# Performance work log

Hardware: AMD Instinct MI355X
Metric: run time of the kernel (lower is better)

The kernel has to match this reference:

```python
import jax, jax.numpy as jnp
import numpy as np

HIDDEN = 1024
INTER = 2816
NUM_EXPERTS = 8
TOP_K = 2
NUM_TASK_EXPERTS = 4
NUM_GENERALISTS = 2
NUM_TASKS = 8
BSZ, SEQ = 4, 2048
NEG = -1e9


def setup_inputs() -> dict:
    key = jax.random.key(0)
    ks = jax.random.split(key, 8)
    s = 1.0 / np.sqrt(HIDDEN)
    si = 1.0 / np.sqrt(INTER)
    return {
        "hidden_states": jax.random.normal(ks[0], (BSZ, SEQ, HIDDEN), jnp.float32),
        "task_id": 3,
        "task_emb": jax.random.normal(ks[1], (NUM_TASKS, HIDDEN), jnp.float32) * 0.02,
        "task_router_w": jax.random.uniform(ks[2], (NUM_EXPERTS, HIDDEN), jnp.float32, -s, s),
        "gate_weight": jax.random.uniform(ks[3], (NUM_EXPERTS, HIDDEN), jnp.float32, -s, s),
        "gate_proj": jax.random.uniform(ks[4], (NUM_EXPERTS, INTER, HIDDEN), jnp.float32, -s, s),
        "up_proj": jax.random.uniform(ks[5], (NUM_EXPERTS, INTER, HIDDEN), jnp.float32, -s, s),
        "down_proj": jax.random.uniform(ks[6], (NUM_EXPERTS, HIDDEN, INTER), jnp.float32, -si, si),
    }


def reference(hidden_states, task_id, task_emb, task_router_w, gate_weight,
              gate_proj, up_proj, down_proj):
    bsz, seq, dim = hidden_states.shape
    E, K = NUM_EXPERTS, TOP_K

    # ---- task-level routing: pick active experts ----
    task_vec = task_emb[task_id]                         # [d]
    task_scores = task_router_w @ task_vec               # [E]
    _, task_idx = jax.lax.top_k(task_scores, NUM_TASK_EXPERTS)
    gen_idx = jnp.arange(E - NUM_GENERALISTS, E)
    active_mask = jnp.zeros((E,), bool).at[task_idx].set(True).at[gen_idx].set(True)

    # ---- token-level gating over active experts (masked full softmax == subset softmax) ----
    gate_input = (hidden_states + task_vec).reshape(-1, dim)      # [N, d]
    logits = gate_input @ gate_weight.T                            # [N, E]
    scores = jax.nn.softmax(jnp.where(active_mask, logits, NEG), axis=-1)
    topk_gates, topk_idx = jax.lax.top_k(scores, K)                # [N, K]
    topk_gates = topk_gates / (topk_gates.sum(-1, keepdims=True) + 1e-6)

    # per-token per-expert combine weight: [N, E]
    comb = (jax.nn.one_hot(topk_idx, E, dtype=topk_gates.dtype) * topk_gates[..., None]).sum(1)

    # ---- expert MLPs (SwiGLU), dense-per-expert then weighted combine ----
    tokens = hidden_states.reshape(-1, dim)                        # [N, d]
    y = jnp.zeros_like(tokens)
    for e in range(E):
        h = jax.nn.silu(tokens @ gate_proj[e].T) * (tokens @ up_proj[e].T)  # [N, I]
        y = y + comb[:, e:e + 1] * (h @ down_proj[e].T)
    return y.reshape(bsz, seq, dim)
```

## Files before the change

### kernel.cpp

```cpp
#include <hip/hip_runtime.h>

#define HIDDEN 1024
#define INTER 2816
#define NE 8
#define NTOK 8192
#define CPAD 32

typedef _Float16 f16;
typedef f16 f16x8 __attribute__((ext_vector_type(8)));
typedef f16 f16x4v __attribute__((ext_vector_type(4)));
typedef float f32x4 __attribute__((ext_vector_type(4)));

typedef __attribute__((address_space(3))) void lds_void;
typedef __attribute__((address_space(1))) void glb_void;

__device__ __forceinline__ void gl_lds16(const void* g, void* l) {
  __builtin_amdgcn_global_load_lds((const glb_void*)g, (lds_void*)l, 16, 0, 0);
}

__device__ __forceinline__ f32x4 mfma16(f16x8 a, f16x8 b, f32x4 c) {
  return __builtin_amdgcn_mfma_f32_16x16x32_f16(a, b, c, 0, 0, 0);
}

__device__ __forceinline__ f16x8 cvt8(float4 a, float4 b) {
  f16x8 v;
  v[0] = (f16)a.x; v[1] = (f16)a.y; v[2] = (f16)a.z; v[3] = (f16)a.w;
  v[4] = (f16)b.x; v[5] = (f16)b.y; v[6] = (f16)b.z; v[7] = (f16)b.w;
  return v;
}

__global__ void k_route(const float* __restrict__ task_emb,
                        const int* __restrict__ task_id_p,
                        const float* __restrict__ trw,
                        int* __restrict__ mask, int* __restrict__ counts) {
  __shared__ float sc[NE];
  const int tid = threadIdx.x;
  counts[tid] = 0;
  const float* tv = task_emb + (size_t)task_id_p[0] * HIDDEN;
  const int e = tid >> 5, l = tid & 31;
  float p = 0.f;
  for (int k = l; k < HIDDEN; k += 32) p += trw[e * HIDDEN + k] * tv[k];
  for (int o = 16; o > 0; o >>= 1) p += __shfl_down(p, o, 32);
  if (l == 0) sc[e] = p;
  __syncthreads();
  if (tid == 0) {
    int m[NE];
    bool used[NE];
    for (int i = 0; i < NE; ++i) { m[i] = 0; used[i] = false; }
    for (int it = 0; it < 4; ++it) {
      float best = -1e30f; int bi = 0;
      for (int i = 0; i < NE; ++i)
        if (!used[i] && sc[i] > best) { best = sc[i]; bi = i; }
      used[bi] = true; m[bi] = 1;
    }
    m[NE - 2] = 1; m[NE - 1] = 1;
    for (int i = 0; i < NE; ++i) mask[i] = m[i];
  }
}

__global__ __launch_bounds__(256) void k_gate(
    const float* __restrict__ x, const float* __restrict__ task_emb,
    const int* __restrict__ task_id_p, const float* __restrict__ gw,
    const int* __restrict__ mask, int* __restrict__ counts,
    int* __restrict__ tok_list, int* __restrict__ tk_e,
    int* __restrict__ tk_pos, float* __restrict__ tk_w,
    f16* __restrict__ X16) {
  const int tid = threadIdx.x;
  const int g = tid >> 3, l8 = tid & 7;
  const int t = blockIdx.x * 32 + g;
  const float4* tv4 = (const float4*)(task_emb + (size_t)task_id_p[0] * HIDDEN);
  const float4* xr4 = (const float4*)(x + (size_t)t * HIDDEN);
  const float4* gw4 = (const float4*)gw;

  float acc[NE];
#pragma unroll
  for (int e = 0; e < NE; ++e) acc[e] = 0.f;
#pragma unroll 4
  for (int it = 0; it < 32; ++it) {
    const int idx4 = it * 8 + l8;
    float4 xv = xr4[idx4];
    f16x4v h4;
    h4[0] = (f16)xv.x; h4[1] = (f16)xv.y; h4[2] = (f16)xv.z; h4[3] = (f16)xv.w;
    *(f16x4v*)(X16 + (size_t)t * HIDDEN + idx4 * 4) = h4;
    float4 tvv = tv4[idx4];
    const float gx = xv.x + tvv.x, gy = xv.y + tvv.y;
    const float gz = xv.z + tvv.z, gwv = xv.w + tvv.w;
#pragma unroll
    for (int e = 0; e < NE; ++e) {
      float4 w = gw4[e * 256 + idx4];
      acc[e] += gx * w.x + gy * w.y + gz * w.z + gwv * w.w;
    }
  }
#pragma unroll
  for (int e = 0; e < NE; ++e) {
    acc[e] += __shfl_down(acc[e], 4, 8);
    acc[e] += __shfl_down(acc[e], 2, 8);
    acc[e] += __shfl_down(acc[e], 1, 8);
  }

  __shared__ int s_e0[32], s_e1[32], s_r0[32], s_r1[32], s_base[NE];
  __shared__ float s_w0[32], s_w1[32];

  if (l8 == 0) {
    float mx = -1e30f;
    for (int e = 0; e < NE; ++e) if (mask[e] && acc[e] > mx) mx = acc[e];
    float pr[NE]; float s = 0.f;
    for (int e = 0; e < NE; ++e) {
      pr[e] = mask[e] ? expf(acc[e] - mx) : 0.f;
      s += pr[e];
    }
    int i0 = 0; float v0 = -1.f;
    for (int e = 0; e < NE; ++e) if (pr[e] > v0) { v0 = pr[e]; i0 = e; }
    int i1 = (i0 == 0) ? 1 : 0; float v1 = -1.f;
    for (int e = 0; e < NE; ++e) if (e != i0 && pr[e] > v1) { v1 = pr[e]; i1 = e; }
    float g0 = v0 / s, g1 = v1 / s;
    float d = g0 + g1 + 1e-6f;
    s_e0[g] = i0; s_e1[g] = i1;
    s_w0[g] = g0 / d; s_w1[g] = g1 / d;
  }
  __syncthreads();
  if (tid == 0) {
    int cnt[NE];
#pragma unroll
    for (int e = 0; e < NE; ++e) cnt[e] = 0;
    for (int i = 0; i < 32; ++i) {
      s_r0[i] = cnt[s_e0[i]]++;
      s_r1[i] = cnt[s_e1[i]]++;
    }
    for (int e = 0; e < NE; ++e)
      s_base[e] = cnt[e] ? atomicAdd(&counts[e * CPAD], cnt[e]) : 0;
  }
  __syncthreads();
  if (l8 == 0) {
    const int e0 = s_e0[g], e1 = s_e1[g];
    const int p0 = s_base[e0] + s_r0[g];
    const int p1 = s_base[e1] + s_r1[g];
    tok_list[e0 * NTOK + p0] = t;
    tok_list[e1 * NTOK + p1] = t;
    tk_e[t] = e0; tk_e[NTOK + t] = e1;
    tk_pos[t] = p0; tk_pos[NTOK + t] = p1;
    tk_w[t] = s_w0[g]; tk_w[NTOK + t] = s_w1[g];
  }
}

__global__ __launch_bounds__(256) void k_wcvt(
    const float* __restrict__ Wg, const float* __restrict__ Wu,
    const float* __restrict__ Wd, const int* __restrict__ mask,
    f16* __restrict__ Wg16, f16* __restrict__ Wu16, f16* __restrict__ Wd16) {
  const int e = blockIdx.z;
  if (!mask[e]) return;
  const int sel = blockIdx.y;
  const float* src = sel == 0 ? Wg : (sel == 1 ? Wu : Wd);
  f16* dst = sel == 0 ? Wg16 : (sel == 1 ? Wu16 : Wd16);
  const size_t i = (size_t)e * INTER * HIDDEN +
                   ((size_t)blockIdx.x * 256 + threadIdx.x) * 8;
  const float4* s4 = (const float4*)(src + i);
  float4 a = s4[0], b = s4[1];
  *(f16x8*)(dst + i) = cvt8(a, b);
}

__global__ __launch_bounds__(256, 2) void k_gateup16(
    const f16* __restrict__ X16, const f16* __restrict__ Wg16,
    const f16* __restrict__ Wu16, const int* __restrict__ counts,
    const int* __restrict__ tok_list, f16* __restrict__ H) {
  const int e = blockIdx.z;
  int ne = 0, pbase = 0;
#pragma unroll
  for (int i = 0; i < NE; ++i) {
    int c = counts[i * CPAD];
    if (i < e) pbase += c;
    if (i == e) ne = c;
  }
  const int m0 = blockIdx.x * 128;
  if (m0 >= ne) return;
  const int n0 = blockIdx.y * 64;

  __shared__ __align__(16) f16 As[128][64];
  __shared__ __align__(16) f16 Bg[64][64];
  __shared__ __align__(16) f16 Bu[64][64];
  __shared__ int toks[128];

  const int tid = threadIdx.x;
  if (tid < 128) {
    int r = m0 + tid;
    toks[tid] = tok_list[e * NTOK + (r < ne ? r : ne - 1)];
  }
  __syncthreads();

  const int row8 = tid >> 3;
  const int sw = ((tid & 7) ^ (row8 & 7)) * 8;
  const f16* asrc[4];
#pragma unroll
  for (int l = 0; l < 4; ++l)
    asrc[l] = X16 + (size_t)toks[l * 32 + row8] * HIDDEN + sw;
  f16* aldst0 = &As[0][0] + tid * 8;
  const size_t ewoff = (size_t)e * INTER * HIDDEN;
  const f16* gsrc0 = Wg16 + ewoff + (size_t)(n0 + row8) * HIDDEN + sw;
  const f16* usrc0 = Wu16 + ewoff + (size_t)(n0 + row8) * HIDDEN + sw;
  f16* gdst0 = &Bg[0][0] + tid * 8;
  f16* udst0 = &Bu[0][0] + tid * 8;

  const int lane = tid & 63;
  const int wave = tid >> 6;
  const int wm = (wave >> 1) * 64;
  const int wn = (wave & 1) * 32;
  const int l15 = lane & 15, grp = lane >> 4;

  const f32x4 zf = {0.f, 0.f, 0.f, 0.f};
  f32x4 accg[4][2], accu[4][2];
#pragma unroll
  for (int i = 0; i < 4; ++i)
#pragma unroll
    for (int j = 0; j < 2; ++j) { accg[i][j] = zf; accu[i][j] = zf; }

#pragma unroll 1
  for (int k0 = 0; k0 < HIDDEN; k0 += 64) {
#pragma unroll
    for (int l = 0; l < 4; ++l)
      gl_lds16(asrc[l] + k0, aldst0 + l * 2048);
    gl_lds16(gsrc0 + k0, gdst0);
    gl_lds16(gsrc0 + k0 + 32 * HIDDEN, gdst0 + 2048);
    gl_lds16(usrc0 + k0, udst0);
    gl_lds16(usrc0 + k0 + 32 * HIDDEN, udst0 + 2048);
    __syncthreads();

#pragma unroll
    for (int h = 0; h < 2; ++h) {
      const int pc = (((h * 4 + grp) ^ (l15 & 7)) << 4);
      f16x8 af[4];
#pragma unroll
      for (int i = 0; i < 4; ++i)
        af[i] = *(const f16x8*)((const char*)&As[0][0] +
                                (wm + i * 16 + l15) * 128 + pc);
      f16x8 bg[2], bu[2];
#pragma unroll
      for (int j = 0; j < 2; ++j) {
        bg[j] = *(const f16x8*)((const char*)&Bg[0][0] +
                                (wn + j * 16 + l15) * 128 + pc);
        bu[j] = *(const f16x8*)((const char*)&Bu[0][0] +
                                (wn + j * 16 + l15) * 128 + pc);
      }
#pragma unroll
      for (int i = 0; i < 4; ++i)
#pragma unroll
        for (int j = 0; j < 2; ++j) {
          accg[i][j] = mfma16(af[i], bg[j], accg[i][j]);
          accu[i][j] = mfma16(af[i], bu[j], accu[i][j]);
        }
    }
    __syncthreads();
  }

  const int col = lane & 15;
  const int quad = lane >> 4;
#pragma unroll
  for (int i = 0; i < 4; ++i)
#pragma unroll
    for (int j = 0; j < 2; ++j)
#pragma unroll
      for (int r = 0; r < 4; ++r) {
        int m = wm + i * 16 + quad * 4 + r;
        if (m0 + m < ne) {
          float gv = accg[i][j][r];
          float uv = accu[i][j][r];
          float hv = (gv / (1.f + expf(-gv))) * uv;
          H[(size_t)(pbase + m0 + m) * INTER + (n0 + wn + j * 16 + col)] = (f16)hv;
        }
      }
}

__global__ __launch_bounds__(256, 2) void k_down16(
    const f16* __restrict__ H, const f16* __restrict__ Wd16,
    const int* __restrict__ counts, f16* __restrict__ Ybuf) {
  const int e = blockIdx.z;
  int ne = 0, pbase = 0;
#pragma unroll
  for (int i = 0; i < NE; ++i) {
    int c = counts[i * CPAD];
    if (i < e) pbase += c;
    if (i == e) ne = c;
  }
  const int m0 = blockIdx.x * 128;
  if (m0 >= ne) return;
  const int n0 = blockIdx.y * 128;

  __shared__ __align__(16) f16 As[128][64];
  __shared__ __align__(16) f16 Bs[128][64];

  const int tid = threadIdx.x;
  const int row8 = tid >> 3;
  const int sw = ((tid & 7) ^ (row8 & 7)) * 8;
  const f16* a0 = H + (size_t)(pbase + m0 + row8) * INTER + sw;
  const f16* b0 = Wd16 + (size_t)e * HIDDEN * INTER +
                  (size_t)(n0 + row8) * INTER + sw;
  f16* aldst0 = &As[0][0] + tid * 8;
  f16* bldst0 = &Bs[0][0] + tid * 8;

  const int lane = tid & 63;
  const int wave = tid >> 6;
  const int wm = (wave >> 1) * 64;
  const int wn = (wave & 1) * 64;
  const int l15 = lane & 15, grp = lane >> 4;

  const f32x4 zf = {0.f, 0.f, 0.f, 0.f};
  f32x4 acc[4][4];
#pragma unroll
  for (int i = 0; i < 4; ++i)
#pragma unroll
    for (int j = 0; j < 4; ++j) acc[i][j] = zf;

#pragma unroll 1
  for (int k0 = 0; k0 < INTER; k0 += 64) {
#pragma unroll
    for (int l = 0; l < 4; ++l) {
      gl_lds16(a0 + (size_t)l * 32 * INTER + k0, aldst0 + l * 2048);
      gl_lds16(b0 + (size_t)l * 32 * INTER + k0, bldst0 + l * 2048);
    }
    __syncthreads();

#pragma unroll
    for (int h = 0; h < 2; ++h) {
      const int pc = (((h * 4 + grp) ^ (l15 & 7)) << 4);
      f16x8 af[4], bf[4];
#pragma unroll
      for (int i = 0; i < 4; ++i)
        af[i] = *(const f16x8*)((const char*)&As[0][0] +
                                (wm + i * 16 + l15) * 128 + pc);
#pragma unroll
      for (int j = 0; j < 4; ++j)
        bf[j] = *(const f16x8*)((const char*)&Bs[0][0] +
                                (wn + j * 16 + l15) * 128 + pc);
#pragma unroll
      for (int i = 0; i < 4; ++i)
#pragma unroll
        for (int j = 0; j < 4; ++j)
          acc[i][j] = mfma16(af[i], bf[j], acc[i][j]);
    }
    __syncthreads();
  }

  const int col = lane & 15;
  const int quad = lane >> 4;
#pragma unroll
  for (int i = 0; i < 4; ++i)
#pragma unroll
    for (int j = 0; j < 4; ++j)
#pragma unroll
      for (int r = 0; r < 4; ++r) {
        int m = wm + i * 16 + quad * 4 + r;
        if (m0 + m < ne)
          Ybuf[(size_t)(pbase + m0 + m) * HIDDEN + (n0 + wn + j * 16 + col)] =
              (f16)acc[i][j][r];
      }
}

__global__ __launch_bounds__(256) void k_combine(
    const f16* __restrict__ Ybuf, const int* __restrict__ tk_e,
    const int* __restrict__ tk_pos, const float* __restrict__ tk_w,
    const int* __restrict__ counts, float* __restrict__ out) {
  __shared__ int s_pre[NE];
  if (threadIdx.x == 0) {
    int p = 0;
    for (int i = 0; i < NE; ++i) { s_pre[i] = p; p += counts[i * CPAD]; }
  }
  __syncthreads();
  const int sub = threadIdx.x >> 7;
  const int t = blockIdx.x * 2 + sub;
  const int c = (threadIdx.x & 127) * 8;
  const int e0 = tk_e[t], e1 = tk_e[NTOK + t];
  const int p0 = s_pre[e0] + tk_pos[t];
  const int p1 = s_pre[e1] + tk_pos[NTOK + t];
  const float w0 = tk_w[t], w1 = tk_w[NTOK + t];
  f16x8 a = *(const f16x8*)(Ybuf + (size_t)p0 * HIDDEN + c);
  f16x8 b = *(const f16x8*)(Ybuf + (size_t)p1 * HIDDEN + c);
  float* o = out + (size_t)t * HIDDEN + c;
  float4 o0, o1;
  o0.x = w0 * (float)a[0] + w1 * (float)b[0];
  o0.y = w0 * (float)a[1] + w1 * (float)b[1];
  o0.z = w0 * (float)a[2] + w1 * (float)b[2];
  o0.w = w0 * (float)a[3] + w1 * (float)b[3];
  o1.x = w0 * (float)a[4] + w1 * (float)b[4];
  o1.y = w0 * (float)a[5] + w1 * (float)b[5];
  o1.z = w0 * (float)a[6] + w1 * (float)b[6];
  o1.w = w0 * (float)a[7] + w1 * (float)b[7];
  *(float4*)o = o0;
  *(float4*)(o + 4) = o1;
}

__global__ void k_sentinel(float* out, float v) {
  int i = blockIdx.x * 256 + threadIdx.x;
  out[i] = v;
}

extern "C" void kernel_launch(void* const* d_in, const int* in_sizes, int n_in,
                              void* d_out, int out_size, void* d_ws, size_t ws_size,
                              hipStream_t stream) {
  const float* x = (const float*)d_in[0];
  const int* task_id = (const int*)d_in[1];
  const float* task_emb = (const float*)d_in[2];
  const float* trw = (const float*)d_in[3];
  const float* gw = (const float*)d_in[4];
  const float* Wg = (const float*)d_in[5];
  const float* Wu = (const float*)d_in[6];
  const float* Wd = (const float*)d_in[7];
  float* out = (float*)d_out;

  char* ws = (char*)d_ws;
  const size_t ROWS_PAD = (size_t)2 * NTOK + 256;
  const size_t IH = (size_t)INTER * HIDDEN;

  size_t off = 0;
  int* mask = (int*)(ws + off); off += 64;
  off = (off + 255) & ~(size_t)255;
  int* counts = (int*)(ws + off); off += NE * CPAD * 4;
  off = (off + 255) & ~(size_t)255;
  int* tk_e = (int*)(ws + off); off += (size_t)2 * NTOK * 4;
  int* tk_pos = (int*)(ws + off); off += (size_t)2 * NTOK * 4;
  float* tk_w = (float*)(ws + off); off += (size_t)2 * NTOK * 4;
  int* tok_list = (int*)(ws + off); off += (size_t)NE * NTOK * 4;
  off = (off + 255) & ~(size_t)255;
  f16* X16 = (f16*)(ws + off); off += (size_t)NTOK * HIDDEN * 2;
  f16* H = (f16*)(ws + off); off += ROWS_PAD * INTER * 2;
  f16* Ybuf = (f16*)(ws + off); off += ROWS_PAD * HIDDEN * 2;
  f16* Wg16 = (f16*)(ws + off); off += (size_t)NE * IH * 2;
  f16* Wu16 = (f16*)(ws + off); off += (size_t)NE * IH * 2;
  f16* Wd16 = (f16*)(ws + off); off += (size_t)NE * IH * 2;
  const size_t need_full = off;

  if (ws_size < need_full) {
    k_sentinel<<<(NTOK * HIDDEN + 255) / 256, 256, 0, stream>>>(
        out, (float)(ws_size >> 20));
    return;
  }

  k_route<<<1, 256, 0, stream>>>(task_emb, task_id, trw, mask, counts);
  k_gate<<<NTOK / 32, 256, 0, stream>>>(x, task_emb, task_id, gw, mask, counts,
                                        tok_list, tk_e, tk_pos, tk_w, X16);
  k_wcvt<<<dim3((unsigned)(IH / (256 * 8)), 3, NE), 256, 0, stream>>>(
      Wg, Wu, Wd, mask, Wg16, Wu16, Wd16);
  k_gateup16<<<dim3(NTOK / 128, INTER / 64, NE), 256, 0, stream>>>(
      X16, Wg16, Wu16, counts, tok_list, H);
  k_down16<<<dim3(NTOK / 128, HIDDEN / 128, NE), 256, 0, stream>>>(
      H, Wd16, counts, Ybuf);
  k_combine<<<NTOK / 2, 256, 0, stream>>>(Ybuf, tk_e, tk_pos, tk_w, counts, out);
}
```

Measured before the change: 726.2 us.

## Fuse gating with weight conversion and compact expert tiles into a tile list

Merges the token gating kernel and the fp32→fp16 weight conversion into a single launch, with extra blocks doing conversion, so both can run concurrently. Adds a small kernel that builds a compact list of (expert, row-tile) work items from the per-expert counts. The grouped GEMM kernels then index that list instead of launching a full tokens×experts grid where most blocks exit early. The grid ordering also changes so N-tiles of one M-tile sit next to each other. The cost is one extra tiny serial kernel launch, plus a fixed MAXTILES grid bound.

```diff
diff --git a/kernel.cpp b/kernel.cpp
--- a/kernel.cpp
+++ b/kernel.cpp
@@ -5,6 +5,7 @@
 #define NE 8
 #define NTOK 8192
 #define CPAD 32
+#define MAXTILES 136
 
 typedef _Float16 f16;
 typedef f16 f16x8 __attribute__((ext_vector_type(8)));
@@ -58,14 +59,32 @@
   }
 }
 
-__global__ __launch_bounds__(256) void k_gate(
+__global__ __launch_bounds__(256) void k_gate_wcvt(
     const float* __restrict__ x, const float* __restrict__ task_emb,
     const int* __restrict__ task_id_p, const float* __restrict__ gw,
     const int* __restrict__ mask, int* __restrict__ counts,
     int* __restrict__ tok_list, int* __restrict__ tk_e,
     int* __restrict__ tk_pos, float* __restrict__ tk_w,
-    f16* __restrict__ X16) {
+    f16* __restrict__ X16,
+    const float* __restrict__ Wg, const float* __restrict__ Wu,
+    const float* __restrict__ Wd,
+    f16* __restrict__ Wg16, f16* __restrict__ Wu16, f16* __restrict__ Wd16) {
   const int tid = threadIdx.x;
+  if (blockIdx.x >= 256) {
+    const int bid = blockIdx.x - 256;
+    const int e = bid / (3 * 1408);
+    const int rem = bid - e * (3 * 1408);
+    const int sel = rem / 1408;
+    const int xb = rem - sel * 1408;
+    if (!mask[e]) return;
+    const float* src = sel == 0 ? Wg : (sel == 1 ? Wu : Wd);
+    f16* dst = sel == 0 ? Wg16 : (sel == 1 ? Wu16 : Wd16);
+    const size_t i = (size_t)e * INTER * HIDDEN + ((size_t)xb * 256 + tid) * 8;
+    const float4* s4 = (const float4*)(src + i);
+    float4 a = s4[0], b = s4[1];
+    *(f16x8*)(dst + i) = cvt8(a, b);
+    return;
+  }
   const int g = tid >> 3, l8 = tid & 7;
   const int t = blockIdx.x * 32 + g;
   const float4* tv4 = (const float4*)(task_emb + (size_t)task_id_p[0] * HIDDEN);
@@ -143,37 +162,34 @@
   }
 }
 
-__global__ __launch_bounds__(256) void k_wcvt(
-    const float* __restrict__ Wg, const float* __restrict__ Wu,
-    const float* __restrict__ Wd, const int* __restrict__ mask,
-    f16* __restrict__ Wg16, f16* __restrict__ Wu16, f16* __restrict__ Wd16) {
-  const int e = blockIdx.z;
-  if (!mask[e]) return;
-  const int sel = blockIdx.y;
-  const float* src = sel == 0 ? Wg : (sel == 1 ? Wu : Wd);
-  f16* dst = sel == 0 ? Wg16 : (sel == 1 ? Wu16 : Wd16);
-  const size_t i = (size_t)e * INTER * HIDDEN +
-                   ((size_t)blockIdx.x * 256 + threadIdx.x) * 8;
-  const float4* s4 = (const float4*)(src + i);
-  float4 a = s4[0], b = s4[1];
-  *(f16x8*)(dst + i) = cvt8(a, b);
+__global__ void k_tiles(const int* __restrict__ counts, int* __restrict__ tiles) {
+  if (threadIdx.x != 0) return;
+  int* te = tiles + 1;
+  int* tm = te + MAXTILES;
+  int* tp = tm + MAXTILES;
+  int* tn = tp + MAXTILES;
+  int p = 0, nt = 0;
+  for (int e = 0; e < NE; ++e) {
+    const int c = counts[e * CPAD];
+    for (int m0 = 0; m0 < c; m0 += 128) {
+      te[nt] = e; tm[nt] = m0; tp[nt] = p; tn[nt] = c; ++nt;
+    }
+    p += c;
+  }
+  tiles[0] = nt;
 }
 
 __global__ __launch_bounds__(256, 2) void k_gateup16(
     const f16* __restrict__ X16, const f16* __restrict__ Wg16,
-    const f16* __restrict__ Wu16, const int* __restrict__ counts,
+    const f16* __restrict__ Wu16, const int* __restrict__ tiles,
     const int* __restrict__ tok_list, f16* __restrict__ H) {
-  const int e = blockIdx.z;
-  int ne = 0, pbase = 0;
-#pragma unroll
-  for (int i = 0; i < NE; ++i) {
-    int c = counts[i * CPAD];
-    if (i < e) pbase += c;
-    if (i == e) ne = c;
-  }
-  const int m0 = blockIdx.x * 128;
-  if (m0 >= ne) return;
-  const int n0 = blockIdx.y * 64;
+  const int yt = blockIdx.y;
+  if (yt >= tiles[0]) return;
+  const int e = tiles[1 + yt];
+  const int m0 = tiles[1 + MAXTILES + yt];
+  const int pbase = tiles[1 + 2 * MAXTILES + yt];
+  const int ne = tiles[1 + 3 * MAXTILES + yt];
+  const int n0 = blockIdx.x * 64;
 
   __shared__ __align__(16) f16 As[128][64];
   __shared__ __align__(16) f16 Bg[64][64];
@@ -271,18 +287,14 @@
 
 __global__ __launch_bounds__(256, 2) void k_down16(
     const f16* __restrict__ H, const f16* __restrict__ Wd16,
-    const int* __restrict__ counts, f16* __restrict__ Ybuf) {
-  const int e = blockIdx.z;
-  int ne = 0, pbase = 0;
-#pragma unroll
-  for (int i = 0; i < NE; ++i) {
-    int c = counts[i * CPAD];
-    if (i < e) pbase += c;
-    if (i == e) ne = c;
-  }
-  const int m0 = blockIdx.x * 128;
-  if (m0 >= ne) return;
-  const int n0 = blockIdx.y * 128;
+    const int* __restrict__ tiles, f16* __restrict__ Ybuf) {
+  const int yt = blockIdx.y;
+  if (yt >= tiles[0]) return;
+  const int e = tiles[1 + yt];
+  const int m0 = tiles[1 + MAXTILES + yt];
+  const int pbase = tiles[1 + 2 * MAXTILES + yt];
+  const int ne = tiles[1 + 3 * MAXTILES + yt];
+  const int n0 = blockIdx.x * 128;
 
   __shared__ __align__(16) f16 As[128][64];
   __shared__ __align__(16) f16 Bs[128][64];
@@ -414,6 +426,8 @@
   off = (off + 255) & ~(size_t)255;
   int* counts = (int*)(ws + off); off += NE * CPAD * 4;
   off = (off + 255) & ~(size_t)255;
+  int* tiles = (int*)(ws + off); off += (1 + 4 * MAXTILES) * 4;
+  off = (off + 255) & ~(size_t)255;
   int* tk_e = (int*)(ws + off); off += (size_t)2 * NTOK * 4;
   int* tk_pos = (int*)(ws + off); off += (size_t)2 * NTOK * 4;
   float* tk_w = (float*)(ws + off); off += (size_t)2 * NTOK * 4;
@@ -434,13 +448,13 @@
   }
 
   k_route<<<1, 256, 0, stream>>>(task_emb, task_id, trw, mask, counts);
-  k_gate<<<NTOK / 32, 256, 0, stream>>>(x, task_emb, task_id, gw, mask, counts,
-                                        tok_list, tk_e, tk_pos, tk_w, X16);
-  k_wcvt<<<dim3((unsigned)(IH / (256 * 8)), 3, NE), 256, 0, stream>>>(
-      Wg, Wu, Wd, mask, Wg16, Wu16, Wd16);
-  k_gateup16<<<dim3(NTOK / 128, INTER / 64, NE), 256, 0, stream>>>(
-      X16, Wg16, Wu16, counts, tok_list, H);
-  k_down16<<<dim3(NTOK / 128, HIDDEN / 128, NE), 256, 0, stream>>>(
-      H, Wd16, counts, Ybuf);
+  k_gate_wcvt<<<256 + 3 * NE * 1408, 256, 0, stream>>>(
+      x, task_emb, task_id, gw, mask, counts, tok_list, tk_e, tk_pos, tk_w,
+      X16, Wg, Wu, Wd, Wg16, Wu16, Wd16);
+  k_tiles<<<1, 64, 0, stream>>>(counts, tiles);
+  k_gateup16<<<dim3(INTER / 64, MAXTILES), 256, 0, stream>>>(
+      X16, Wg16, Wu16, tiles, tok_list, H);
+  k_down16<<<dim3(HIDDEN / 128, MAXTILES), 256, 0, stream>>>(
+      H, Wd16, tiles, Ybuf);
   k_combine<<<NTOK / 2, 256, 0, stream>>>(Ybuf, tk_e, tk_pos, tk_w, counts, out);
 }
```

After: 659.0 us. -9.3%, faster.
